# Performance work log

Measured on AMD Instinct MI355X. Metric: run time of the kernel, lower is better.

## Reference

```python
import jax, jax.numpy as jnp
import numpy as np

C = 512       # out_channels
RATIO = 2
K = C // RATIO          # init_channels = 256
NEW = K * (RATIO - 1)   # new_channels = 256
H = W = 160
EPS = 1e-5


def _conv(x, w, pad, groups=1):
    return jax.lax.conv_general_dilated(
        x, w, (1, 1), [(pad, pad), (pad, pad)],
        dimension_numbers=("NCHW", "OIHW", "NCHW"),
        feature_group_count=groups)


def _bn(x, g, b, m, v):
    scale = (g / jnp.sqrt(v + EPS))[None, :, None, None]
    return (x - m[None, :, None, None]) * scale + b[None, :, None, None]


def setup_inputs() -> dict:
    key = jax.random.key(0)
    ks = jax.random.split(key, 16)
    s = 0.05
    return {
        "x": jax.random.normal(ks[0], (1, C, H, W), jnp.float32),
        "w_fc1": jax.random.normal(ks[1], (K, C), jnp.float32) * s,
        "w_fc2": jax.random.normal(ks[2], (C, K), jnp.float32) * s,
        "w_cheap": jax.random.normal(ks[3], (NEW, 1, 3, 3), jnp.float32) * s,  # depthwise, groups=K
        "bn1_g": jnp.ones((NEW,), jnp.float32),
        "bn1_b": jnp.zeros((NEW,), jnp.float32),
        "bn1_m": jax.random.normal(ks[4], (NEW,), jnp.float32) * s,
        "bn1_v": jax.random.uniform(ks[5], (NEW,), jnp.float32, 0.5, 1.5),
        "w_dc1": jax.random.normal(ks[6], (C, 2 * C, 1, 1), jnp.float32) * s,
        "b_dc1": jax.random.normal(ks[7], (C,), jnp.float32) * s,
        "bn2_g": jnp.ones((C,), jnp.float32),
        "bn2_b": jnp.zeros((C,), jnp.float32),
        "bn2_m": jax.random.normal(ks[8], (C,), jnp.float32) * s,
        "bn2_v": jax.random.uniform(ks[9], (C,), jnp.float32, 0.5, 1.5),
        "w_dc2": jax.random.normal(ks[10], (C, C, 3, 3), jnp.float32) * s,
        "b_dc2": jax.random.normal(ks[11], (C,), jnp.float32) * s,
    }


def reference(x, w_fc1, w_fc2, w_cheap, bn1_g, bn1_b, bn1_m, bn1_v,
              w_dc1, b_dc1, bn2_g, bn2_b, bn2_m, bn2_v, w_dc2, b_dc2):
    # ---- channel attention (CBAM-style shared MLP over avg+max pool) ----
    avg = x.mean(axis=(2, 3))                      # [1, C]
    mx = x.max(axis=(2, 3))                        # [1, C]
    mlp = lambda p: jax.nn.relu(p @ w_fc1.T) @ w_fc2.T
    scales = jax.nn.sigmoid(mlp(avg) + mlp(mx))    # [1, C]
    # ---- sort-based top-K channel select, kept in channel-index order ----
    # torch: sort desc, drop channels ranked >= K via boolean mask (mask is in
    # channel-index order), equivalent to gathering sorted top-K indices.
    _, top_idx = jax.lax.top_k(scales[0], K)
    idx = jnp.sort(top_idx)
    x1 = x[:, idx]                                 # [1, K, H, W]
    # ---- cheap operation: depthwise 3x3 + BN + ReLU ----
    x2 = jax.nn.relu(_bn(_conv(x1, w_cheap, 1, groups=K), bn1_g, bn1_b, bn1_m, bn1_v))
    # ---- concat [x*scales, x1, x2] -> 2C channels ----
    cat = jnp.concatenate([x * scales[:, :, None, None], x1, x2], axis=1)
    # ---- down_channel: 1x1 conv + BN + 3x3 conv + ReLU ----
    h = _conv(cat, w_dc1, 0) + b_dc1[None, :, None, None]
    h = _bn(h, bn2_g, bn2_b, bn2_m, bn2_v)
    h = _conv(h, w_dc2, 1) + b_dc2[None, :, None, None]
    return jax.nn.relu(h)
```

## Files before the change

kernel.cpp:

```cpp
#include <hip/hip_runtime.h>
#include <math.h>

#define C 512
#define K 256
#define HW 160
#define NPIX (HW*HW)
#define PW 162
#define EPS 1e-5f

typedef __attribute__((ext_vector_type(8))) short s16x8;
typedef __attribute__((ext_vector_type(16))) float f32x16;

__device__ __forceinline__ unsigned short f2bf(float f) {
    unsigned int u = __float_as_uint(f);
    u += 0x7fffu + ((u >> 16) & 1u);
    return (unsigned short)(u >> 16);
}

__device__ __forceinline__ void ldg_lds16(const void* g, void* l) {
    __builtin_amdgcn_global_load_lds((const __attribute__((address_space(1))) unsigned int*)g,
                                     (__attribute__((address_space(3))) unsigned int*)l, 16, 0, 0);
}

#define WAIT_VM0()   asm volatile("s_waitcnt vmcnt(0)" ::: "memory")
#define WAIT_VM10()  asm volatile("s_waitcnt vmcnt(10)" ::: "memory")

__global__ void reduce_kernel(const float* __restrict__ x,
                              float* __restrict__ avg, float* __restrict__ mx) {
    int c = blockIdx.x;
    const float4* xc = (const float4*)(x + (size_t)c * NPIX);
    float s = 0.f, m = -INFINITY;
    for (int p = threadIdx.x; p < NPIX / 4; p += 256) {
        float4 v = xc[p];
        s += v.x + v.y + v.z + v.w;
        m = fmaxf(m, fmaxf(fmaxf(v.x, v.y), fmaxf(v.z, v.w)));
    }
    __shared__ float ss[256], sm[256];
    ss[threadIdx.x] = s; sm[threadIdx.x] = m;
    __syncthreads();
    for (int o = 128; o > 0; o >>= 1) {
        if (threadIdx.x < o) {
            ss[threadIdx.x] += ss[threadIdx.x + o];
            sm[threadIdx.x] = fmaxf(sm[threadIdx.x], sm[threadIdx.x + o]);
        }
        __syncthreads();
    }
    if (threadIdx.x == 0) {
        avg[c] = ss[0] / (float)NPIX;
        mx[c]  = sm[0];
    }
}

__global__ void mlp_select_kernel(const float* __restrict__ avg,
                                  const float* __restrict__ mx,
                                  const float* __restrict__ w_fc1,
                                  const float* __restrict__ w_fc2,
                                  float* __restrict__ scales_out,
                                  int* __restrict__ idx,
                                  int* __restrict__ pos) {
    __shared__ float s_avg[C], s_mx[C], s_h[K], s_scales[C];
    __shared__ int s_sel[C];
    int t = threadIdx.x;
    s_avg[t] = avg[t];
    s_mx[t]  = mx[t];
    __syncthreads();
    if (t < K) {
        float ha = 0.f, hm = 0.f;
        const float4* wr = (const float4*)(w_fc1 + (size_t)t * C);
        for (int c = 0; c < C / 4; c++) {
            float4 w = wr[c];
            ha += s_avg[4*c]*w.x + s_avg[4*c+1]*w.y + s_avg[4*c+2]*w.z + s_avg[4*c+3]*w.w;
            hm += s_mx[4*c]*w.x + s_mx[4*c+1]*w.y + s_mx[4*c+2]*w.z + s_mx[4*c+3]*w.w;
        }
        s_h[t] = fmaxf(ha, 0.f) + fmaxf(hm, 0.f);
    }
    __syncthreads();
    {
        float o = 0.f;
        const float4* wr = (const float4*)(w_fc2 + (size_t)t * K);
        for (int k = 0; k < K / 4; k++) {
            float4 w = wr[k];
            o += s_h[4*k]*w.x + s_h[4*k+1]*w.y + s_h[4*k+2]*w.z + s_h[4*k+3]*w.w;
        }
        float sc = 1.f / (1.f + expf(-o));
        s_scales[t] = sc;
        scales_out[t] = sc;
    }
    __syncthreads();
    {
        float v = s_scales[t];
        int rank = 0;
        for (int i = 0; i < C; i++) {
            float u = s_scales[i];
            rank += (u > v) || (u == v && i < t);
        }
        s_sel[t] = (rank < K) ? 1 : 0;
    }
    __syncthreads();
    {
        int p = 0;
        for (int i = 0; i < t; i++) p += s_sel[i];
        if (s_sel[t]) { idx[p] = t; pos[t] = p; }
        else pos[t] = -1;
    }
}

__global__ void prep_kernel(const float* __restrict__ w_dc2, unsigned short* __restrict__ w3f,
                            const float* __restrict__ w_dc1, const float* __restrict__ scales,
                            const int* __restrict__ pos, unsigned short* __restrict__ wAf,
                            unsigned short* __restrict__ hpad,
                            const float* __restrict__ b_dc1,
                            const float* __restrict__ g2, const float* __restrict__ b2,
                            const float* __restrict__ m2, const float* __restrict__ v2,
                            float* __restrict__ scale2, float* __restrict__ shift2) {
    int b = blockIdx.x;
    if (b < 384) {
        int g = b / 48, ph = b % 48;
        int dy = ph >> 4, kc = ph & 15;
        for (int u = threadIdx.x; u < 6144; u += 256) {
            int chunk = u >> 9;
            int dx = chunk >> 2, j = (chunk >> 1) & 1, s = chunk & 1;
            int r = u & 511, lane = r >> 3, e = r & 7;
            int co = g * 64 + j * 32 + (lane & 31);
            int qq = lane >> 5;
            int ci = kc * 32 + (s * 2 + qq) * 8 + e;
            w3f[(size_t)b * 6144 + u] = f2bf(w_dc2[((size_t)co * 512 + ci) * 9 + dy * 3 + dx]);
        }
    } else if (b < 576) {
        int bb = b - 384;
        int g = bb / 24, ph = bb % 24;
        for (int u = threadIdx.x; u < 2048; u += 256) {
            int chunk = u >> 9;
            int j = chunk >> 1, s = chunk & 1;
            int r = u & 511, lane = r >> 3, e = r & 7;
            int co = g * 64 + j * 32 + (lane & 31);
            int qq = lane >> 5;
            int c = ph * 32 + (s * 2 + qq) * 8 + e;
            const float* wr = w_dc1 + (size_t)co * 1024;
            float v;
            if (c < 512) {
                v = wr[c] * scales[c];
                int pp = pos[c];
                if (pp >= 0) v += wr[512 + pp];
            } else {
                v = wr[768 + (c - 512)];
            }
            wAf[(size_t)bb * 2048 + u] = f2bf(v);
        }
    } else if (b < 737) {
        int t = (b - 576) * 256 + threadIdx.x;
        int pix = t >> 6;
        int p;
        if (pix < 162)      p = pix;
        else if (pix < 324) p = 161 * PW + (pix - 162);
        else {
            int r = pix - 324;
            p = (1 + (r >> 1)) * PW + ((r & 1) ? 161 : 0);
        }
        *(uint4*)&hpad[(size_t)p * 512 + (t & 63) * 8] = make_uint4(0u, 0u, 0u, 0u);
    } else {
        for (int c = threadIdx.x; c < C; c += 256) {
            float s = g2[c] * rsqrtf(v2[c] + EPS);
            scale2[c] = s;
            shift2[c] = (b_dc1[c] - m2[c]) * s + b2[c];
        }
    }
}

__global__ void dw_t_kernel(const float* __restrict__ x,
                            const int* __restrict__ idx,
                            const float* __restrict__ wch,
                            const float* __restrict__ g1, const float* __restrict__ b1,
                            const float* __restrict__ m1, const float* __restrict__ v1,
                            unsigned short* __restrict__ xcat) {
    __shared__ float tile[32][33];
    int tx = threadIdx.x & 31, ty = threadIdx.x >> 5;
    int pbase = blockIdx.x * 32, kbase = blockIdx.y * 32;
    int y = pbase / HW, x0 = pbase % HW;
    int px = x0 + tx;
#pragma unroll
    for (int jj = 0; jj < 4; jj++) {
        int k = kbase + ty + jj * 8;
        int c = idx[k];
        const float* xc = x + (size_t)c * NPIX;
        const float* wk = wch + k * 9;
        float acc = 0.f;
#pragma unroll
        for (int dy = 0; dy < 3; dy++) {
            int yy = y + dy - 1;
            if (yy < 0 || yy >= HW) continue;
#pragma unroll
            for (int dx = 0; dx < 3; dx++) {
                int xv = px + dx - 1;
                if (xv < 0 || xv >= HW) continue;
                acc += xc[yy * HW + xv] * wk[dy * 3 + dx];
            }
        }
        float s = g1[k] * rsqrtf(v1[k] + EPS);
        tile[ty + jj * 8][tx] = fmaxf((acc - m1[k]) * s + b1[k], 0.f);
    }
    __syncthreads();
#pragma unroll
    for (int jj = 0; jj < 4; jj++) {
        int p = pbase + ty + jj * 8;
        xcat[(size_t)p * 768 + 512 + kbase + tx] = f2bf(tile[tx][ty + jj * 8]);
    }
}

__global__ void transpose_kernel(const float* __restrict__ x,
                                 unsigned short* __restrict__ xcat) {
    __shared__ float tile[32][33];
    int tx = threadIdx.x & 31, ty = threadIdx.x >> 5;
    int pbase = blockIdx.x * 32, cbase = blockIdx.y * 32;
#pragma unroll
    for (int j = 0; j < 4; j++) {
        int c = cbase + ty + j * 8;
        tile[ty + j * 8][tx] = x[(size_t)c * NPIX + pbase + tx];
    }
    __syncthreads();
#pragma unroll
    for (int j = 0; j < 4; j++) {
        int p = pbase + ty + j * 8;
        xcat[(size_t)p * 768 + cbase + tx] = f2bf(tile[tx][ty + j * 8]);
    }
}

__global__ __launch_bounds__(64, 1) void conv1_mfma(const unsigned short* __restrict__ xcat,
        const unsigned short* __restrict__ wAf,
        const float* __restrict__ scale2, const float* __restrict__ shift2,
        unsigned short* __restrict__ hpad) {
    __shared__ unsigned short Al[3][640 * 8];
    int y = blockIdx.x, g = blockIdx.y, co0 = g * 64;
    int lane = threadIdx.x;
    int l31 = lane & 31, q = lane >> 5;
    f32x16 acc[5][2] = {};

    int aoff[10];
#pragma unroll
    for (int r = 0; r < 10; r++) {
        int gg = r * 64 + lane;
        int px = gg >> 2, jg = (gg & 3) ^ ((px >> 1) & 3);
        aoff[r] = px * 768 + jg * 8;
    }
    int raoff[2];
#pragma unroll
    for (int s = 0; s < 2; s++)
        raoff[s] = l31 * 64 + (((s * 2 + q) ^ ((l31 >> 1) & 3)) << 4);
    const unsigned short* arow = xcat + (size_t)y * HW * 768;
    const s16x8* bbase = (const s16x8*)wAf + ((size_t)g * 24) * 256 + lane;

    auto stageA = [&](int ph, int buf) {
        int kc = ph * 32;
        unsigned short* An = Al[buf];
#pragma unroll
        for (int r = 0; r < 10; r++) ldg_lds16(arow + kc + aoff[r], &An[r * 512]);
    };

    stageA(0, 0);
    stageA(1, 1);
    for (int ph = 0; ph < 24; ph++) {
        const unsigned short* Ar = Al[ph % 3];
        if (ph == 23) { WAIT_VM0(); } else { WAIT_VM10(); }
        const s16x8* bp = bbase + (size_t)ph * 256;
        s16x8 bf[2][2];
#pragma unroll
        for (int j = 0; j < 2; j++)
#pragma unroll
            for (int s = 0; s < 2; s++)
                bf[j][s] = bp[(j * 2 + s) * 64];
        s16x8 af[5][2];
#pragma unroll
        for (int s = 0; s < 2; s++)
#pragma unroll
            for (int i = 0; i < 5; i++)
                af[i][s] = *(const s16x8*)((const char*)Ar + i * 2048 + raoff[s]);
        if (ph < 22) stageA(ph + 2, (ph + 2) % 3);
#pragma unroll
        for (int s = 0; s < 2; s++)
#pragma unroll
            for (int i = 0; i < 5; i++)
#pragma unroll
                for (int j = 0; j < 2; j++)
                    acc[i][j] = __builtin_amdgcn_mfma_f32_32x32x16_bf16(af[i][s], bf[j][s], acc[i][j], 0, 0, 0);
    }
#pragma unroll
    for (int j = 0; j < 2; j++) {
        int co = co0 + j * 32 + l31;
        float s2 = scale2[co], sh = shift2[co];
#pragma unroll
        for (int i = 0; i < 5; i++) {
#pragma unroll
            for (int rg = 0; rg < 4; rg++) {
#pragma unroll
                for (int t = 0; t < 4; t++) {
                    int px = i * 32 + t + rg * 8 + q * 4;
                    size_t pp = (size_t)(y + 1) * PW + px + 1;
                    hpad[pp * 512 + co] = f2bf(acc[i][j][rg * 4 + t] * s2 + sh);
                }
            }
        }
    }
}

__global__ __launch_bounds__(64, 1) void conv3_mfma(const unsigned short* __restrict__ hpad,
        const unsigned short* __restrict__ w3f,
        const float* __restrict__ bias, float* __restrict__ out) {
    __shared__ unsigned short Al[2][648 * 8];
    int y = blockIdx.x, g = blockIdx.y, co0 = g * 64;
    int lane = threadIdx.x;
    int l31 = lane & 31, q = lane >> 5;
    f32x16 acc[5][2] = {};

    int aoff[11];
#pragma unroll
    for (int r = 0; r < 11; r++) {
        int gg = r * 64 + lane;
        int px = gg >> 2, jg = (gg & 3) ^ ((px >> 1) & 3);
        aoff[r] = px * 512 + jg * 8;
    }
    int raoff[3][2];
#pragma unroll
    for (int dx = 0; dx < 3; dx++)
#pragma unroll
        for (int s = 0; s < 2; s++) {
            int m = l31 + dx;
            raoff[dx][s] = m * 64 + ((((s * 2 + q)) ^ ((m >> 1) & 3)) << 4);
        }
    const s16x8* bbase = (const s16x8*)w3f + ((size_t)g * 48) * 768 + lane;

    auto stageA = [&](int ph, int buf) {
        int dy = ph >> 4, kc = (ph & 15) * 32;
        const unsigned short* ab = hpad + ((size_t)(y + dy) * PW) * 512 + kc;
        unsigned short* An = Al[buf];
#pragma unroll
        for (int r = 0; r < 10; r++) ldg_lds16(ab + aoff[r], &An[r * 512]);
        if (lane < 8)                ldg_lds16(ab + aoff[10], &An[10 * 512]);
    };

    stageA(0, 0);
    for (int ph = 0; ph < 48; ph++) {
        const unsigned short* Ar = Al[ph & 1];
        WAIT_VM0();
        const s16x8* bp = bbase + (size_t)ph * 768;
        s16x8 bf[3][2][2];
#pragma unroll
        for (int dx = 0; dx < 3; dx++)
#pragma unroll
            for (int j = 0; j < 2; j++)
#pragma unroll
                for (int s = 0; s < 2; s++)
                    bf[dx][j][s] = bp[(dx * 4 + j * 2 + s) * 64];
#pragma unroll
        for (int dx = 0; dx < 3; dx++) {
            s16x8 af[5][2];
#pragma unroll
            for (int s = 0; s < 2; s++)
#pragma unroll
                for (int i = 0; i < 5; i++)
                    af[i][s] = *(const s16x8*)((const char*)Ar + i * 2048 + raoff[dx][s]);
            if (dx == 0 && ph < 47) stageA(ph + 1, (ph + 1) & 1);
#pragma unroll
            for (int s = 0; s < 2; s++)
#pragma unroll
                for (int i = 0; i < 5; i++)
#pragma unroll
                    for (int j = 0; j < 2; j++)
                        acc[i][j] = __builtin_amdgcn_mfma_f32_32x32x16_bf16(af[i][s], bf[dx][j][s], acc[i][j], 0, 0, 0);
        }
    }
#pragma unroll
    for (int j = 0; j < 2; j++) {
        int co = co0 + j * 32 + l31;
        float b = bias[co];
        float* op = out + (size_t)co * NPIX + y * HW;
#pragma unroll
        for (int i = 0; i < 5; i++) {
#pragma unroll
            for (int rg = 0; rg < 4; rg++) {
                int px = i * 32 + rg * 8 + q * 4;
                float4 v;
                v.x = fmaxf(acc[i][j][rg * 4 + 0] + b, 0.f);
                v.y = fmaxf(acc[i][j][rg * 4 + 1] + b, 0.f);
                v.z = fmaxf(acc[i][j][rg * 4 + 2] + b, 0.f);
                v.w = fmaxf(acc[i][j][rg * 4 + 3] + b, 0.f);
                *(float4*)&op[px] = v;
            }
        }
    }
}

extern "C" void kernel_launch(void* const* d_in, const int* in_sizes, int n_in,
                              void* d_out, int out_size, void* d_ws, size_t ws_size,
                              hipStream_t stream) {
    const float* x      = (const float*)d_in[0];
    const float* w_fc1  = (const float*)d_in[1];
    const float* w_fc2  = (const float*)d_in[2];
    const float* w_ch   = (const float*)d_in[3];
    const float* bn1_g  = (const float*)d_in[4];
    const float* bn1_b  = (const float*)d_in[5];
    const float* bn1_m  = (const float*)d_in[6];
    const float* bn1_v  = (const float*)d_in[7];
    const float* w_dc1  = (const float*)d_in[8];
    const float* b_dc1  = (const float*)d_in[9];
    const float* bn2_g  = (const float*)d_in[10];
    const float* bn2_b  = (const float*)d_in[11];
    const float* bn2_m  = (const float*)d_in[12];
    const float* bn2_v  = (const float*)d_in[13];
    const float* w_dc2  = (const float*)d_in[14];
    const float* b_dc2  = (const float*)d_in[15];
    float* out = (float*)d_out;

    char* ws = (char*)d_ws;
    float* avg    = (float*)(ws + 0);
    float* mx     = (float*)(ws + 2048);
    float* scales = (float*)(ws + 4096);
    int*   idx    = (int*)  (ws + 6144);
    int*   pos    = (int*)  (ws + 7168);
    float* scale2 = (float*)(ws + 9216);
    float* shift2 = (float*)(ws + 11264);
    unsigned short* wAf  = (unsigned short*)(ws + 16384);
    unsigned short* w3f  = (unsigned short*)(ws + 802816);
    unsigned short* xcat = (unsigned short*)(ws + 31735808);
    unsigned short* hpad = (unsigned short*)(ws + 71057408);

    reduce_kernel<<<C, 256, 0, stream>>>(x, avg, mx);
    mlp_select_kernel<<<1, C, 0, stream>>>(avg, mx, w_fc1, w_fc2, scales, idx, pos);
    prep_kernel<<<738, 256, 0, stream>>>(w_dc2, w3f, w_dc1, scales, pos, wAf, hpad,
                                         b_dc1, bn2_g, bn2_b, bn2_m, bn2_v, scale2, shift2);
    dw_t_kernel<<<dim3(800, 8), 256, 0, stream>>>(x, idx, w_ch, bn1_g, bn1_b, bn1_m, bn1_v, xcat);
    transpose_kernel<<<dim3(800, 16), 256, 0, stream>>>(x, xcat);
    conv1_mfma<<<dim3(HW, 8), 64, 0, stream>>>(xcat, wAf, scale2, shift2, hpad);
    conv3_mfma<<<dim3(HW, 8), 64, 0, stream>>>(hpad, w3f, b_dc2, out);
}
```

Before: 476.2 us.

## Prefetch B fragments two phases ahead and triple-buffer conv3 A tiles

```diff
diff --git a/kernel.cpp b/kernel.cpp
--- a/kernel.cpp
+++ b/kernel.cpp
@@ -23,7 +23,8 @@
 }
 
 #define WAIT_VM0()   asm volatile("s_waitcnt vmcnt(0)" ::: "memory")
-#define WAIT_VM10()  asm volatile("s_waitcnt vmcnt(10)" ::: "memory")
+#define WAIT_VM14()  asm volatile("s_waitcnt vmcnt(14)" ::: "memory")
+#define WAIT_VM23()  asm volatile("s_waitcnt vmcnt(23)" ::: "memory")
 
 __global__ void reduce_kernel(const float* __restrict__ x,
                               float* __restrict__ avg, float* __restrict__ mx) {
@@ -230,7 +231,7 @@
         const float* __restrict__ scale2, const float* __restrict__ shift2,
         unsigned short* __restrict__ hpad) {
     __shared__ unsigned short Al[3][640 * 8];
-    int y = blockIdx.x, g = blockIdx.y, co0 = g * 64;
+    int g = blockIdx.x, y = blockIdx.y, co0 = g * 64;
     int lane = threadIdx.x;
     int l31 = lane & 31, q = lane >> 5;
     f32x16 acc[5][2] = {};
@@ -255,19 +256,20 @@
 #pragma unroll
         for (int r = 0; r < 10; r++) ldg_lds16(arow + kc + aoff[r], &An[r * 512]);
     };
-
-    stageA(0, 0);
-    stageA(1, 1);
+    s16x8 bfb[2][2][2];
+    auto loadB = [&](int ph, int sel) {
+#pragma unroll
+        for (int j = 0; j < 2; j++)
+#pragma unroll
+            for (int s = 0; s < 2; s++)
+                bfb[sel][j][s] = bbase[(size_t)ph * 256 + (j * 2 + s) * 64];
+    };
+
+    stageA(0, 0); loadB(0, 0);
+    stageA(1, 1); loadB(1, 1);
     for (int ph = 0; ph < 24; ph++) {
         const unsigned short* Ar = Al[ph % 3];
-        if (ph == 23) { WAIT_VM0(); } else { WAIT_VM10(); }
-        const s16x8* bp = bbase + (size_t)ph * 256;
-        s16x8 bf[2][2];
-#pragma unroll
-        for (int j = 0; j < 2; j++)
-#pragma unroll
-            for (int s = 0; s < 2; s++)
-                bf[j][s] = bp[(j * 2 + s) * 64];
+        if (ph == 23) { WAIT_VM0(); } else { WAIT_VM14(); }
         s16x8 af[5][2];
 #pragma unroll
         for (int s = 0; s < 2; s++)
@@ -275,13 +277,15 @@
             for (int i = 0; i < 5; i++)
                 af[i][s] = *(const s16x8*)((const char*)Ar + i * 2048 + raoff[s]);
         if (ph < 22) stageA(ph + 2, (ph + 2) % 3);
+        int sel = ph & 1;
 #pragma unroll
         for (int s = 0; s < 2; s++)
 #pragma unroll
             for (int i = 0; i < 5; i++)
 #pragma unroll
                 for (int j = 0; j < 2; j++)
-                    acc[i][j] = __builtin_amdgcn_mfma_f32_32x32x16_bf16(af[i][s], bf[j][s], acc[i][j], 0, 0, 0);
+                    acc[i][j] = __builtin_amdgcn_mfma_f32_32x32x16_bf16(af[i][s], bfb[sel][j][s], acc[i][j], 0, 0, 0);
+        if (ph < 22) loadB(ph + 2, sel);
     }
 #pragma unroll
     for (int j = 0; j < 2; j++) {
@@ -305,8 +309,8 @@
 __global__ __launch_bounds__(64, 1) void conv3_mfma(const unsigned short* __restrict__ hpad,
         const unsigned short* __restrict__ w3f,
         const float* __restrict__ bias, float* __restrict__ out) {
-    __shared__ unsigned short Al[2][648 * 8];
-    int y = blockIdx.x, g = blockIdx.y, co0 = g * 64;
+    __shared__ unsigned short Al[3][648 * 8];
+    int g = blockIdx.x, y = blockIdx.y, co0 = g * 64;
     int lane = threadIdx.x;
     int l31 = lane & 31, q = lane >> 5;
     f32x16 acc[5][2] = {};
@@ -336,20 +340,23 @@
         for (int r = 0; r < 10; r++) ldg_lds16(ab + aoff[r], &An[r * 512]);
         if (lane < 8)                ldg_lds16(ab + aoff[10], &An[10 * 512]);
     };
-
-    stageA(0, 0);
+    s16x8 bfb[2][3][2][2];
+    auto loadB = [&](int ph, int sel) {
+#pragma unroll
+        for (int dx = 0; dx < 3; dx++)
+#pragma unroll
+            for (int j = 0; j < 2; j++)
+#pragma unroll
+                for (int s = 0; s < 2; s++)
+                    bfb[sel][dx][j][s] = bbase[(size_t)ph * 768 + (dx * 4 + j * 2 + s) * 64];
+    };
+
+    stageA(0, 0); loadB(0, 0);
+    stageA(1, 1); loadB(1, 1);
     for (int ph = 0; ph < 48; ph++) {
-        const unsigned short* Ar = Al[ph & 1];
-        WAIT_VM0();
-        const s16x8* bp = bbase + (size_t)ph * 768;
-        s16x8 bf[3][2][2];
-#pragma unroll
-        for (int dx = 0; dx < 3; dx++)
-#pragma unroll
-            for (int j = 0; j < 2; j++)
-#pragma unroll
-                for (int s = 0; s < 2; s++)
-                    bf[dx][j][s] = bp[(dx * 4 + j * 2 + s) * 64];
+        const unsigned short* Ar = Al[ph % 3];
+        if (ph == 47) { WAIT_VM0(); } else { WAIT_VM23(); }
+        int sel = ph & 1;
 #pragma unroll
         for (int dx = 0; dx < 3; dx++) {
             s16x8 af[5][2];
@@ -358,15 +365,16 @@
 #pragma unroll
                 for (int i = 0; i < 5; i++)
                     af[i][s] = *(const s16x8*)((const char*)Ar + i * 2048 + raoff[dx][s]);
-            if (dx == 0 && ph < 47) stageA(ph + 1, (ph + 1) & 1);
+            if (dx == 0 && ph < 46) stageA(ph + 2, (ph + 2) % 3);
 #pragma unroll
             for (int s = 0; s < 2; s++)
 #pragma unroll
                 for (int i = 0; i < 5; i++)
 #pragma unroll
                     for (int j = 0; j < 2; j++)
-                        acc[i][j] = __builtin_amdgcn_mfma_f32_32x32x16_bf16(af[i][s], bf[dx][j][s], acc[i][j], 0, 0, 0);
-        }
+                        acc[i][j] = __builtin_amdgcn_mfma_f32_32x32x16_bf16(af[i][s], bfb[sel][dx][j][s], acc[i][j], 0, 0, 0);
+        }
+        if (ph < 46) loadB(ph + 2, sel);
     }
 #pragma unroll
     for (int j = 0; j < 2; j++) {
@@ -429,6 +437,6 @@
                                          b_dc1, bn2_g, bn2_b, bn2_m, bn2_v, scale2, shift2);
     dw_t_kernel<<<dim3(800, 8), 256, 0, stream>>>(x, idx, w_ch, bn1_g, bn1_b, bn1_m, bn1_v, xcat);
     transpose_kernel<<<dim3(800, 16), 256, 0, stream>>>(x, xcat);
-    conv1_mfma<<<dim3(HW, 8), 64, 0, stream>>>(xcat, wAf, scale2, shift2, hpad);
-    conv3_mfma<<<dim3(HW, 8), 64, 0, stream>>>(hpad, w3f, b_dc2, out);
-}
+    conv1_mfma<<<dim3(8, HW), 64, 0, stream>>>(xcat, wAf, scale2, shift2, hpad);
+    conv3_mfma<<<dim3(8, HW), 64, 0, stream>>>(hpad, w3f, b_dc2, out);
+}
```

Result: slower. 795.4 us (+67.0%).
